# Performance work log

Measured on AMD Instinct MI355X. Metric: run time of the kernel, lower is better.

## Reference

```python
import jax, jax.numpy as jnp
import numpy as np

B, T, U, V = 8, 512, 128, 128  # batch, frames, label len (U+1 pred steps), vocab incl. blank
BLANK = 0


def setup_inputs() -> dict:
    key = jax.random.key(0)
    k1, k2, k3, k4 = jax.random.split(key, 4)
    logits = jax.random.normal(k1, (B, T, U + 1, V), dtype=jnp.float32)
    y = jax.random.randint(k2, (B, U), 1, V).astype(jnp.int32)  # labels, never blank
    logit_lens = jax.random.randint(k3, (B,), T // 2, T + 1).astype(jnp.int32)
    y_lens = jax.random.randint(k4, (B,), U // 2, U + 1).astype(jnp.int32)
    batch_offset = jnp.cumsum(logit_lens * (y_lens + 1)).astype(jnp.int32)
    return {
        "logits": logits,
        "y": y,
        "logit_lens": logit_lens,
        "y_lens": y_lens,
        "batch_offset": batch_offset,
        "max_f_len": T,
    }


def _combine(e1, e2):
    # log-domain affine recurrence x[u] = logaddexp(x[u-1] + c[u], a[u])
    c1, a1 = e1
    c2, a2 = e2
    return (c1 + c2, jnp.logaddexp(a1 + c2, a2))


def rnnt_loss(logits, y, logit_lens, y_lens, blank_idx):
    Bb, Tt, U1, Vv = logits.shape
    Uu = U1 - 1
    lp = jax.nn.log_softmax(logits, axis=-1)            # [B,T,U+1,V]
    blank = lp[..., blank_idx]                          # [B,T,U+1]
    idx = jnp.broadcast_to(y[:, None, :, None], (Bb, Tt, Uu, 1)).astype(jnp.int32)
    emit = jnp.take_along_axis(lp[:, :, :Uu, :], idx, axis=3)[..., 0]  # [B,T,U]

    # alpha[0,u] = sum_{v<u} emit(0,v)
    row0 = jnp.concatenate(
        [jnp.zeros((Bb, 1), lp.dtype), jnp.cumsum(emit[:, 0, :], axis=1)], axis=1
    )  # [B,U+1]
    neg = jnp.full((Bb, 1), -jnp.inf, lp.dtype)

    def step(prev_row, x):
        bl_prev, em_t = x                               # [B,U+1], [B,U]
        a = prev_row + bl_prev                          # come-from-below (blank at t-1)
        c = jnp.concatenate([neg, em_t], axis=1)        # come-from-left (emit at t)
        _, row = jax.lax.associative_scan(_combine, (c, a), axis=1)
        return row, row

    xs = (jnp.swapaxes(blank[:, : Tt - 1, :], 0, 1), jnp.swapaxes(emit[:, 1:, :], 0, 1))
    _, rows = jax.lax.scan(step, row0, xs)              # [T-1,B,U+1]
    alphas = jnp.swapaxes(jnp.concatenate([row0[None], rows], axis=0), 0, 1)  # [B,T,U+1]

    bi = jnp.arange(Bb)
    ti = logit_lens - 1
    ui = y_lens
    ll = alphas[bi, ti, ui] + blank[bi, ti, ui]
    return -ll                                          # per-utterance negative log-lik


def reference(logits, y, logit_lens, y_lens, batch_offset, max_f_len):
    # batch_offset / max_f_len are packing metadata, unused when packed_input=False
    return rnnt_loss(logits, y, logit_lens, y_lens, BLANK).mean()
```

## Files before the change

kernel.cpp:

```cpp
#include <hip/hip_runtime.h>

#define Bb 8
#define Tt 512
#define Uu 128
#define U1 129
#define Vv 128

#define OUT_OFF 0
#define CTROWS 321
#define PCKROW 512
#define PCKBSZ ((size_t)CTROWS * PCKROW)
#define PCK_OFF ((size_t)Bb * Tt * U1 * 2)
#define CTCOL_OFF (PCK_OFF + (size_t)Bb * PCKBSZ)
#define RES_OFF (CTCOL_OFF + (size_t)Bb * CTROWS * 4)

#define K_LN2    0.6931471805599453f
#define K_INVLN2 1.4426950408889634f
#define SENT (-1.0e30f)

__device__ __forceinline__ float fexp2(float x) {
    float r; asm("v_exp_f32 %0, %1" : "=v"(r) : "v"(x)); return r;
}
__device__ __forceinline__ float flog2(float x) {
    float r; asm("v_log_f32 %0, %1" : "=v"(r) : "v"(x)); return r;
}
__device__ __forceinline__ float fmax3(float x, float y, float z) {
    float r; asm("v_max3_f32 %0, %1, %2, %3" : "=v"(r) : "v"(x), "v"(y), "v"(z));
    return r;
}

__global__ __launch_bounds__(256) void lse_kernel(
    const float* __restrict__ logits, const int* __restrict__ y,
    const int* __restrict__ logit_lens, const int* __restrict__ y_lens,
    float* __restrict__ ws)
{
    const int b = blockIdx.y;
    const int t = blockIdx.x;
    if (t >= logit_lens[b]) return;
    const int Ue = y_lens[b];

    float2* outv = (float2*)(ws + OUT_OFF);
    const int wid  = threadIdx.x >> 6;
    const int lane = threadIdx.x & 63;
    const int g    = lane >> 4;
    const int gl   = lane & 15;
    const unsigned rowbase = ((unsigned)b * Tt + t) * U1;
    const int yb = b * Uu;

    for (int u0 = wid * 8; u0 <= Ue; u0 += 32) {
        const int ua = u0 + g;
        const int ub = u0 + 4 + g;
        const int uca = ua > Ue ? Ue : ua;
        const int ucb = ub > Ue ? Ue : ub;
        const float* pa = logits + (size_t)(rowbase + uca) * Vv;
        const float* pb = logits + (size_t)(rowbase + ucb) * Vv;
        float4 a1 = *(const float4*)(pa + gl * 4);
        float4 a2 = *(const float4*)(pa + 64 + gl * 4);
        float4 b1 = *(const float4*)(pb + gl * 4);
        float4 b2 = *(const float4*)(pb + 64 + gl * 4);

        float sa = (fexp2(a1.x * K_INVLN2) + fexp2(a1.y * K_INVLN2))
                 + (fexp2(a1.z * K_INVLN2) + fexp2(a1.w * K_INVLN2))
                 + (fexp2(a2.x * K_INVLN2) + fexp2(a2.y * K_INVLN2))
                 + (fexp2(a2.z * K_INVLN2) + fexp2(a2.w * K_INVLN2));
        float sb = (fexp2(b1.x * K_INVLN2) + fexp2(b1.y * K_INVLN2))
                 + (fexp2(b1.z * K_INVLN2) + fexp2(b1.w * K_INVLN2))
                 + (fexp2(b2.x * K_INVLN2) + fexp2(b2.y * K_INVLN2))
                 + (fexp2(b2.z * K_INVLN2) + fexp2(b2.w * K_INVLN2));
        #pragma unroll
        for (int off = 8; off; off >>= 1) {
            sa += __shfl_xor(sa, off);
            sb += __shfl_xor(sb, off);
        }
        float lseA = flog2(sa);
        float lseB = flog2(sb);

        float emA = SENT, emB = SENT;
        if (uca < Uu) {
            int yv = y[yb + uca];
            int c = yv & 3;
            float4 cv = (yv & 64) ? a2 : a1;
            float cand = (c == 0) ? cv.x : (c == 1) ? cv.y : (c == 2) ? cv.z : cv.w;
            float ev = __shfl(cand, (lane & 48) | ((yv & 63) >> 2));
            emA = ev * K_INVLN2 - lseA;
        }
        if (ucb < Uu) {
            int yv = y[yb + ucb];
            int c = yv & 3;
            float4 cv = (yv & 64) ? b2 : b1;
            float cand = (c == 0) ? cv.x : (c == 1) ? cv.y : (c == 2) ? cv.z : cv.w;
            float ev = __shfl(cand, (lane & 48) | ((yv & 63) >> 2));
            emB = ev * K_INVLN2 - lseB;
        }
        if (gl == 0) {
            if (ua <= Ue) outv[rowbase + ua] = make_float2(a1.x * K_INVLN2 - lseA, emA);
            if (ub <= Ue) outv[rowbase + ub] = make_float2(b1.x * K_INVLN2 - lseB, emB);
        }
    }
}

__device__ __forceinline__ float lae2(float x, float y) {
    float dd = x - y;
    float nad = __builtin_bit_cast(float, __builtin_bit_cast(int, dd) | 0x80000000);
    return fmaxf(x, y) + flog2(1.0f + fexp2(nad));
}
__device__ __forceinline__ float lae3(float x, float y, float z) {
    float m = fmax3(x, y, z);
    return m + flog2(fexp2(x - m) + fexp2(y - m) + fexp2(z - m));
}

__global__ __launch_bounds__(256) void cond_kernel(
    const int* __restrict__ logit_lens, const int* __restrict__ y_lens,
    float* __restrict__ ws)
{
    const int b = blockIdx.x / 320;
    const int m = blockIdx.x - b * 320 + 1;
    if (m > ((logit_lens[b] - 1 + y_lens[b]) >> 1)) return;
    const int r1 = 2 * m - 2, r2 = 2 * m - 1;
    const float2* outv = (const float2*)(ws + OUT_OFF);

    __shared__ float2 D1[U1], D2[U1];
    __shared__ float pckS[PCKROW];
    for (int q = threadIdx.x; q < 2 * U1; q += 256) {
        const int which = q >= U1;
        const int j = q - which * U1;
        const int t = (which ? r2 : r1) - j;
        float2 val = make_float2(SENT, SENT);
        if (t >= 0 && t < Tt) val = outv[((size_t)b * Tt + t) * U1 + j];
        (which ? D2 : D1)[j] = val;
    }
    __syncthreads();

    const int u = threadIdx.x;
    if (u <= 128) {
        float2 d1  = D1[u], d2 = D2[u];
        float2 d1m = (u >= 1) ? D1[u - 1] : make_float2(SENT, SENT);
        float d2my  = (u >= 1) ? D2[u - 1].y : SENT;
        float d1m2y = (u >= 2) ? D1[u - 2].y : SENT;
        float A = d1.x + d2.x;
        float B = lae2(d1m.y + d2.x, d1m.x + d2my);
        float C = d1m2y + d2my;
        if (u < 128) {
            int base = (u >> 1) * 8 + (u & 1);
            pckS[base]     = A;
            pckS[base + 2] = B;
            pckS[base + 4] = C;
            if ((u & 1) == 0) { pckS[base + 6] = 0.0f; pckS[base + 7] = 0.0f; }
        } else {
            ((float4*)(ws + CTCOL_OFF))[(size_t)b * CTROWS + m] = make_float4(A, B, C, 0.0f);
        }
    }
    __syncthreads();

    float* pckG = ws + PCK_OFF + (size_t)b * PCKBSZ + (size_t)m * PCKROW;
    for (int i = threadIdx.x; i < PCKROW; i += 256) pckG[i] = pckS[i];
}

template<int MODE>
__device__ __forceinline__ float rot1(float x, int lane) {
    if constexpr (MODE == 2) {
        float s = __shfl_up(x, 1);
        float w = __shfl(x, 63);
        return (lane == 0) ? w : s;
    } else {
        constexpr int CTRL = (MODE == 0) ? 0x13C : 0x134;
        int i = __builtin_bit_cast(int, x);
        i = __builtin_amdgcn_update_dpp(i, i, CTRL, 0xF, 0xF, true);
        return __builtin_bit_cast(float, i);
    }
}

template<int MODE, bool H128>
__device__ __forceinline__ void dp_body(int b, int lane, int Tb, int Ub,
                                        float* __restrict__ ws)
{
    const float2* outv = (const float2*)(ws + OUT_OFF);
    const float* PCKb = ws + PCK_OFF + (size_t)b * PCKBSZ;
    const float4* COLb = (const float4*)(ws + CTCOL_OFF) + (size_t)b * CTROWS;
    int zv; asm volatile("v_mov_b32 %0, 0" : "=v"(zv));

    float px = (lane == 0) ? 0.0f : SENT;
    float py = SENT, p2 = SENT;
    const int dend = Tb - 1 + Ub;
    const int np   = dend >> 1;
    const int odd  = dend & 1;

    float2 F1 = make_float2(0,0), F2 = make_float2(0,0), G = make_float2(0,0);
    if (odd) {
        const int r = dend - 1;
        int j1 = 2 * lane, j2 = 2 * lane + 1;
        int t1 = r - j1; t1 = t1 > Tt - 1 ? Tt - 1 : t1;
        int t2 = r - j2; t2 = t2 > Tt - 1 ? Tt - 1 : t2;
        F1 = outv[((size_t)b * Tt + t1) * U1 + j1];
        F2 = outv[((size_t)b * Tt + t2) * U1 + j2];
        if constexpr (H128) G = outv[((size_t)b * Tt + (r - 128)) * U1 + 128];
    }
    float pbf = outv[((size_t)b * Tt + (Tb - 1)) * U1 + Ub + zv].x;

    float4 Q0,Q1,Q2,Q3,Q4,Q5,Q6,Q7,Q8,Q9,Q10,Q11,Q12,Q13,Q14,Q15;
    float2 R0,R1,R2,R3,R4,R5,R6,R7,R8,R9,R10,R11,R12,R13,R14,R15;
    float4 O0,O1,O2,O3,O4,O5,O6,O7,O8,O9,O10,O11,O12,O13,O14,O15;

#define LOADC(i, mm) { unsigned o = (unsigned)(mm) * PCKROW + (lane << 3); \
    Q##i = *(const float4*)(PCKb + o); \
    R##i = *(const float2*)(PCKb + o + 4); \
    if constexpr (H128) O##i = COLb[(mm) + zv]; }

#define PIN(i) if constexpr (H128) { \
        asm volatile("" : "+v"(Q##i.x), "+v"(Q##i.y), "+v"(Q##i.z), "+v"(Q##i.w), \
                          "+v"(R##i.x), "+v"(R##i.y), "+v"(O##i.x), "+v"(O##i.y), "+v"(O##i.z)); \
    } else { \
        asm volatile("" : "+v"(Q##i.x), "+v"(Q##i.y), "+v"(Q##i.z), "+v"(Q##i.w), \
                          "+v"(R##i.x), "+v"(R##i.y)); \
    }

#define COMP2(i) { \
    float pm1 = rot1<MODE>(py, lane); \
    float pm0 = rot1<MODE>(px, lane); \
    float nx = lae3(px + Q##i.x, pm1 + Q##i.z, pm0 + R##i.x); \
    float ny = lae3(py + Q##i.y, px + Q##i.w, pm1 + R##i.y); \
    if constexpr (H128) p2 = lae3(p2 + O##i.x, pm1 + O##i.y, pm0 + O##i.z); \
    px = nx; py = ny; }

    LOADC(0,1)   LOADC(1,2)   LOADC(2,3)   LOADC(3,4)
    LOADC(4,5)   LOADC(5,6)   LOADC(6,7)   LOADC(7,8)
    LOADC(8,9)   LOADC(9,10)  LOADC(10,11) LOADC(11,12)
    LOADC(12,13) LOADC(13,14) LOADC(14,15) LOADC(15,16)

    int m = 1;
    for (; m + 15 <= np; m += 16) {
        PIN(0)  COMP2(0)  { int dn = m + 16 > np ? np : m + 16; LOADC(0,  dn) }
        PIN(1)  COMP2(1)  { int dn = m + 17 > np ? np : m + 17; LOADC(1,  dn) }
        PIN(2)  COMP2(2)  { int dn = m + 18 > np ? np : m + 18; LOADC(2,  dn) }
        PIN(3)  COMP2(3)  { int dn = m + 19 > np ? np : m + 19; LOADC(3,  dn) }
        PIN(4)  COMP2(4)  { int dn = m + 20 > np ? np : m + 20; LOADC(4,  dn) }
        PIN(5)  COMP2(5)  { int dn = m + 21 > np ? np : m + 21; LOADC(5,  dn) }
        PIN(6)  COMP2(6)  { int dn = m + 22 > np ? np : m + 22; LOADC(6,  dn) }
        PIN(7)  COMP2(7)  { int dn = m + 23 > np ? np : m + 23; LOADC(7,  dn) }
        PIN(8)  COMP2(8)  { int dn = m + 24 > np ? np : m + 24; LOADC(8,  dn) }
        PIN(9)  COMP2(9)  { int dn = m + 25 > np ? np : m + 25; LOADC(9,  dn) }
        PIN(10) COMP2(10) { int dn = m + 26 > np ? np : m + 26; LOADC(10, dn) }
        PIN(11) COMP2(11) { int dn = m + 27 > np ? np : m + 27; LOADC(11, dn) }
        PIN(12) COMP2(12) { int dn = m + 28 > np ? np : m + 28; LOADC(12, dn) }
        PIN(13) COMP2(13) { int dn = m + 29 > np ? np : m + 29; LOADC(13, dn) }
        PIN(14) COMP2(14) { int dn = m + 30 > np ? np : m + 30; LOADC(14, dn) }
        PIN(15) COMP2(15) { int dn = m + 31 > np ? np : m + 31; LOADC(15, dn) }
    }
#define TAILC(i) if (m <= np) { PIN(i) COMP2(i) m++; }
    TAILC(0)  TAILC(1)  TAILC(2)  TAILC(3)  TAILC(4)
    TAILC(5)  TAILC(6)  TAILC(7)  TAILC(8)  TAILC(9)
    TAILC(10) TAILC(11) TAILC(12) TAILC(13) TAILC(14)

    if (odd) {
        float pm  = rot1<MODE>(py, lane);
        float pmE = rot1<MODE>(F2.y, lane);
        float pmE0 = (lane == 0) ? SENT : pmE;
        float nx = lae2(px + F1.x, pm + pmE0);
        float ny = lae2(py + F2.x, px + F1.y);
        if constexpr (H128) p2 = lae2(p2 + G.x, pm + pmE);
        px = nx; py = ny;
    }

    float a;
    if constexpr (H128) {
        a = __shfl(p2, 0);
    } else {
        float ax = __shfl(px, Ub >> 1);
        float ay = __shfl(py, Ub >> 1);
        a = (Ub & 1) ? ay : ax;
    }
    if (lane == 0) {
        ws[RES_OFF + b] = -(a + pbf) * K_LN2;
    }
#undef LOADC
#undef PIN
#undef COMP2
#undef TAILC
}

__global__ __launch_bounds__(64) void dp_kernel(
    const int* __restrict__ logit_lens, const int* __restrict__ y_lens,
    float* __restrict__ ws)
{
    const int b = blockIdx.x;
    const int lane = threadIdx.x;
    const int Tb = logit_lens[b];
    const int Ub = y_lens[b];
    const bool h = (Ub == 128);
    int li = lane;
    int r0 = __builtin_amdgcn_update_dpp(li, li, 0x13C , 0xF, 0xF, true);
    int r1 = __builtin_amdgcn_update_dpp(li, li, 0x134 , 0xF, 0xF, true);
    int want = (lane + 63) & 63;
    if (__all(r0 == want)) {
        if (h) dp_body<0, true>(b, lane, Tb, Ub, ws);
        else   dp_body<0, false>(b, lane, Tb, Ub, ws);
    } else if (__all(r1 == want)) {
        if (h) dp_body<1, true>(b, lane, Tb, Ub, ws);
        else   dp_body<1, false>(b, lane, Tb, Ub, ws);
    } else {
        if (h) dp_body<2, true>(b, lane, Tb, Ub, ws);
        else   dp_body<2, false>(b, lane, Tb, Ub, ws);
    }
}

__global__ void mean_kernel(const float* __restrict__ res, float* __restrict__ out)
{
    if (threadIdx.x == 0) {
        float s = 0.0f;
        #pragma unroll
        for (int i = 0; i < Bb; ++i) s += res[i];
        out[0] = s * (1.0f / Bb);
    }
}

extern "C" void kernel_launch(void* const* d_in, const int* in_sizes, int n_in,
                              void* d_out, int out_size, void* d_ws, size_t ws_size,
                              hipStream_t stream) {
    const float* logits     = (const float*)d_in[0];
    const int*   y          = (const int*)d_in[1];
    const int*   logit_lens = (const int*)d_in[2];
    const int*   y_lens     = (const int*)d_in[3];
    float* ws  = (float*)d_ws;
    float* out = (float*)d_out;

    dim3 lgrid(Tt, Bb);
    lse_kernel<<<lgrid, 256, 0, stream>>>(logits, y, logit_lens, y_lens, ws);
    cond_kernel<<<Bb * 320, 256, 0, stream>>>(logit_lens, y_lens, ws);
    dp_kernel<<<Bb, 64, 0, stream>>>(logit_lens, y_lens, ws);
    mean_kernel<<<1, 64, 0, stream>>>(ws + RES_OFF, out);
}
```

Before: 69.45 us.

## Compose pairs of diagonal transition matrices to halve serial DP steps

Adds a compose_kernel that multiplies consecutive pairs of banded two-diagonal transition operators in the log-semiring, producing a five-band operator per four anti-diagonals. The serial single-wave DP then advances four diagonals per step using lae5 and two-lane rotations instead of two diagonals with lae3, which shortens the latency-bound sequential chain. In exchange it adds another kernel launch, more workspace traffic and more per-step transcendental work, and the tail handling now covers leftover two-diagonal and odd steps.

```diff
diff --git a/kernel.cpp b/kernel.cpp
--- a/kernel.cpp
+++ b/kernel.cpp
@@ -12,7 +12,12 @@
 #define PCKBSZ ((size_t)CTROWS * PCKROW)
 #define PCK_OFF ((size_t)Bb * Tt * U1 * 2)
 #define CTCOL_OFF (PCK_OFF + (size_t)Bb * PCKBSZ)
-#define RES_OFF (CTCOL_OFF + (size_t)Bb * CTROWS * 4)
+#define WROWF 768
+#define WROWS 160
+#define WBSZ ((size_t)WROWS * WROWF)
+#define W_OFF (CTCOL_OFF + (size_t)Bb * CTROWS * 4)
+#define WCOL_OFF (W_OFF + (size_t)Bb * WBSZ)
+#define RES_OFF (WCOL_OFF + (size_t)Bb * WROWS * 8)
 
 #define K_LN2    0.6931471805599453f
 #define K_INVLN2 1.4426950408889634f
@@ -107,6 +112,12 @@
 __device__ __forceinline__ float lae3(float x, float y, float z) {
     float m = fmax3(x, y, z);
     return m + flog2(fexp2(x - m) + fexp2(y - m) + fexp2(z - m));
+}
+__device__ __forceinline__ float lae5(float a, float b, float c, float d, float e) {
+    float m = fmax3(a, b, c);
+    m = fmax3(m, d, e);
+    return m + flog2(fexp2(a - m) + fexp2(b - m) + fexp2(c - m)
+                   + fexp2(d - m) + fexp2(e - m));
 }
 
 __global__ __launch_bounds__(256) void cond_kernel(
@@ -156,6 +167,70 @@
     for (int i = threadIdx.x; i < PCKROW; i += 256) pckG[i] = pckS[i];
 }
 
+__global__ __launch_bounds__(256) void compose_kernel(
+    const int* __restrict__ logit_lens, const int* __restrict__ y_lens,
+    float* __restrict__ ws)
+{
+    const int b = blockIdx.x / 159;
+    const int q = blockIdx.x - b * 159 + 1;
+    const int dend = logit_lens[b] - 1 + y_lens[b];
+    if (4 * q > dend) return;
+    const int m1 = 2 * q - 1, m2 = 2 * q;
+    const float* PCKb = ws + PCK_OFF + (size_t)b * PCKBSZ;
+    const float4* COLb = (const float4*)(ws + CTCOL_OFF) + (size_t)b * CTROWS;
+
+    __shared__ float a1s[131], b1s[131], c1s[131];
+    __shared__ float wrk[WROWF];
+    const int u = threadIdx.x;
+    if (u < 2) { a1s[u] = SENT; b1s[u] = SENT; c1s[u] = SENT; }
+    if (u < 128) {
+        const float* p = PCKb + (size_t)m1 * PCKROW + (u >> 1) * 8;
+        int par = u & 1;
+        a1s[u + 2] = p[par]; b1s[u + 2] = p[2 + par]; c1s[u + 2] = p[4 + par];
+    } else if (u == 128) {
+        float4 cc = COLb[m1];
+        a1s[130] = cc.x; b1s[130] = cc.y; c1s[130] = cc.z;
+    }
+    __syncthreads();
+
+    if (u <= 128) {
+        float A2, B2, C2;
+        if (u < 128) {
+            const float* p = PCKb + (size_t)m2 * PCKROW + (u >> 1) * 8;
+            int par = u & 1;
+            A2 = p[par]; B2 = p[2 + par]; C2 = p[4 + par];
+        } else {
+            float4 cc = COLb[m2];
+            A2 = cc.x; B2 = cc.y; C2 = cc.z;
+        }
+        float A1 = a1s[u + 2], A1m = a1s[u + 1], A1m2 = a1s[u];
+        float B1 = b1s[u + 2], B1m = b1s[u + 1], B1m2 = b1s[u];
+        float C1 = c1s[u + 2], C1m = c1s[u + 1], C1m2 = c1s[u];
+        float W0 = A2 + A1;
+        float W1 = lae2(A2 + B1, B2 + A1m);
+        float W2 = lae3(A2 + C1, B2 + B1m, C2 + A1m2);
+        float W3 = lae2(B2 + C1m, C2 + B1m2);
+        float W4 = C2 + C1m2;
+        if (u < 128) {
+            int base = (u >> 1) * 12 + (u & 1);
+            wrk[base]     = W0;
+            wrk[base + 2] = W1;
+            wrk[base + 4] = W2;
+            wrk[base + 6] = W3;
+            wrk[base + 8] = W4;
+            if ((u & 1) == 0) { wrk[base + 10] = 0.0f; wrk[base + 11] = 0.0f; }
+        } else {
+            float* wc = ws + WCOL_OFF + ((size_t)b * WROWS + q) * 8;
+            wc[0] = W0; wc[1] = W1; wc[2] = W2; wc[3] = W3; wc[4] = W4;
+            wc[5] = 0.0f; wc[6] = 0.0f; wc[7] = 0.0f;
+        }
+    }
+    __syncthreads();
+
+    float* wg = ws + W_OFF + (size_t)b * WBSZ + (size_t)q * WROWF;
+    for (int i = threadIdx.x; i < WROWF; i += 256) wg[i] = wrk[i];
+}
+
 template<int MODE>
 __device__ __forceinline__ float rot1(float x, int lane) {
     if constexpr (MODE == 2) {
@@ -177,16 +252,24 @@
     const float2* outv = (const float2*)(ws + OUT_OFF);
     const float* PCKb = ws + PCK_OFF + (size_t)b * PCKBSZ;
     const float4* COLb = (const float4*)(ws + CTCOL_OFF) + (size_t)b * CTROWS;
+    const float* WTb = ws + W_OFF + (size_t)b * WBSZ;
+    const float* WCb = ws + WCOL_OFF + (size_t)b * WROWS * 8;
     int zv; asm volatile("v_mov_b32 %0, 0" : "=v"(zv));
 
     float px = (lane == 0) ? 0.0f : SENT;
     float py = SENT, p2 = SENT;
     const int dend = Tb - 1 + Ub;
-    const int np   = dend >> 1;
-    const int odd  = dend & 1;
+    const int nq   = dend >> 2;
+    const int rem  = dend & 3;
+
+    const int mpair = 2 * nq + 1;
+    float4 Qp = *(const float4*)(PCKb + (size_t)mpair * PCKROW + (lane << 3));
+    float2 Rp = *(const float2*)(PCKb + (size_t)mpair * PCKROW + (lane << 3) + 4);
+    float4 Op = make_float4(SENT, SENT, SENT, 0.0f);
+    if constexpr (H128) Op = COLb[mpair + zv];
 
     float2 F1 = make_float2(0,0), F2 = make_float2(0,0), G = make_float2(0,0);
-    if (odd) {
+    if (rem & 1) {
         const int r = dend - 1;
         int j1 = 2 * lane, j2 = 2 * lane + 1;
         int t1 = r - j1; t1 = t1 > Tt - 1 ? Tt - 1 : t1;
@@ -197,61 +280,69 @@
     }
     float pbf = outv[((size_t)b * Tt + (Tb - 1)) * U1 + Ub + zv].x;
 
-    float4 Q0,Q1,Q2,Q3,Q4,Q5,Q6,Q7,Q8,Q9,Q10,Q11,Q12,Q13,Q14,Q15;
-    float2 R0,R1,R2,R3,R4,R5,R6,R7,R8,R9,R10,R11,R12,R13,R14,R15;
-    float4 O0,O1,O2,O3,O4,O5,O6,O7,O8,O9,O10,O11,O12,O13,O14,O15;
-
-#define LOADC(i, mm) { unsigned o = (unsigned)(mm) * PCKROW + (lane << 3); \
-    Q##i = *(const float4*)(PCKb + o); \
-    R##i = *(const float2*)(PCKb + o + 4); \
-    if constexpr (H128) O##i = COLb[(mm) + zv]; }
+    float4 A0,A1,A2,A3,A4,A5,A6,A7;
+    float4 B0,B1,B2,B3,B4,B5,B6,B7;
+    float2 C0,C1,C2,C3,C4,C5,C6,C7;
+    float4 Oa0,Oa1,Oa2,Oa3,Oa4,Oa5,Oa6,Oa7;
+    float2 Oc0,Oc1,Oc2,Oc3,Oc4,Oc5,Oc6,Oc7;
+
+#define LOADW(i, qq) { unsigned o = (unsigned)(qq) * WROWF + lane * 12; \
+    A##i = *(const float4*)(WTb + o); \
+    B##i = *(const float4*)(WTb + o + 4); \
+    C##i = *(const float2*)(WTb + o + 8); \
+    if constexpr (H128) { \
+        Oa##i = *(const float4*)(WCb + (qq) * 8 + zv); \
+        Oc##i = *(const float2*)(WCb + (qq) * 8 + 4 + zv); } }
 
 #define PIN(i) if constexpr (H128) { \
-        asm volatile("" : "+v"(Q##i.x), "+v"(Q##i.y), "+v"(Q##i.z), "+v"(Q##i.w), \
-                          "+v"(R##i.x), "+v"(R##i.y), "+v"(O##i.x), "+v"(O##i.y), "+v"(O##i.z)); \
+        asm volatile("" : "+v"(A##i.x), "+v"(A##i.y), "+v"(A##i.z), "+v"(A##i.w), \
+                          "+v"(B##i.x), "+v"(B##i.y), "+v"(B##i.z), "+v"(B##i.w), \
+                          "+v"(C##i.x), "+v"(C##i.y), \
+                          "+v"(Oa##i.x), "+v"(Oa##i.y), "+v"(Oa##i.z), "+v"(Oa##i.w), \
+                          "+v"(Oc##i.x)); \
     } else { \
-        asm volatile("" : "+v"(Q##i.x), "+v"(Q##i.y), "+v"(Q##i.z), "+v"(Q##i.w), \
-                          "+v"(R##i.x), "+v"(R##i.y)); \
-    }
-
-#define COMP2(i) { \
-    float pm1 = rot1<MODE>(py, lane); \
-    float pm0 = rot1<MODE>(px, lane); \
-    float nx = lae3(px + Q##i.x, pm1 + Q##i.z, pm0 + R##i.x); \
-    float ny = lae3(py + Q##i.y, px + Q##i.w, pm1 + R##i.y); \
-    if constexpr (H128) p2 = lae3(p2 + O##i.x, pm1 + O##i.y, pm0 + O##i.z); \
+        asm volatile("" : "+v"(A##i.x), "+v"(A##i.y), "+v"(A##i.z), "+v"(A##i.w), \
+                          "+v"(B##i.x), "+v"(B##i.y), "+v"(B##i.z), "+v"(B##i.w), \
+                          "+v"(C##i.x), "+v"(C##i.y)); \
+    }
+
+#define COMP4(i) { \
+    float p1y = rot1<MODE>(py, lane); \
+    float p1x = rot1<MODE>(px, lane); \
+    float p2y = rot1<MODE>(p1y, lane); \
+    float p2x = rot1<MODE>(p1x, lane); \
+    float nx = lae5(px + A##i.x, p1y + A##i.z, p1x + B##i.x, p2y + B##i.z, p2x + C##i.x); \
+    float ny = lae5(py + A##i.y, px + A##i.w, p1y + B##i.y, p1x + B##i.w, p2y + C##i.y); \
+    if constexpr (H128) p2 = lae5(p2 + Oa##i.x, p1y + Oa##i.y, p1x + Oa##i.z, \
+                                  p2y + Oa##i.w, p2x + Oc##i.x); \
     px = nx; py = ny; }
 
-    LOADC(0,1)   LOADC(1,2)   LOADC(2,3)   LOADC(3,4)
-    LOADC(4,5)   LOADC(5,6)   LOADC(6,7)   LOADC(7,8)
-    LOADC(8,9)   LOADC(9,10)  LOADC(10,11) LOADC(11,12)
-    LOADC(12,13) LOADC(13,14) LOADC(14,15) LOADC(15,16)
-
-    int m = 1;
-    for (; m + 15 <= np; m += 16) {
-        PIN(0)  COMP2(0)  { int dn = m + 16 > np ? np : m + 16; LOADC(0,  dn) }
-        PIN(1)  COMP2(1)  { int dn = m + 17 > np ? np : m + 17; LOADC(1,  dn) }
-        PIN(2)  COMP2(2)  { int dn = m + 18 > np ? np : m + 18; LOADC(2,  dn) }
-        PIN(3)  COMP2(3)  { int dn = m + 19 > np ? np : m + 19; LOADC(3,  dn) }
-        PIN(4)  COMP2(4)  { int dn = m + 20 > np ? np : m + 20; LOADC(4,  dn) }
-        PIN(5)  COMP2(5)  { int dn = m + 21 > np ? np : m + 21; LOADC(5,  dn) }
-        PIN(6)  COMP2(6)  { int dn = m + 22 > np ? np : m + 22; LOADC(6,  dn) }
-        PIN(7)  COMP2(7)  { int dn = m + 23 > np ? np : m + 23; LOADC(7,  dn) }
-        PIN(8)  COMP2(8)  { int dn = m + 24 > np ? np : m + 24; LOADC(8,  dn) }
-        PIN(9)  COMP2(9)  { int dn = m + 25 > np ? np : m + 25; LOADC(9,  dn) }
-        PIN(10) COMP2(10) { int dn = m + 26 > np ? np : m + 26; LOADC(10, dn) }
-        PIN(11) COMP2(11) { int dn = m + 27 > np ? np : m + 27; LOADC(11, dn) }
-        PIN(12) COMP2(12) { int dn = m + 28 > np ? np : m + 28; LOADC(12, dn) }
-        PIN(13) COMP2(13) { int dn = m + 29 > np ? np : m + 29; LOADC(13, dn) }
-        PIN(14) COMP2(14) { int dn = m + 30 > np ? np : m + 30; LOADC(14, dn) }
-        PIN(15) COMP2(15) { int dn = m + 31 > np ? np : m + 31; LOADC(15, dn) }
-    }
-#define TAILC(i) if (m <= np) { PIN(i) COMP2(i) m++; }
-    TAILC(0)  TAILC(1)  TAILC(2)  TAILC(3)  TAILC(4)
-    TAILC(5)  TAILC(6)  TAILC(7)  TAILC(8)  TAILC(9)
-    TAILC(10) TAILC(11) TAILC(12) TAILC(13) TAILC(14)
-
-    if (odd) {
+    LOADW(0,1) LOADW(1,2) LOADW(2,3) LOADW(3,4)
+    LOADW(4,5) LOADW(5,6) LOADW(6,7) LOADW(7,8)
+
+    int q = 1;
+    for (; q + 7 <= nq; q += 8) {
+        PIN(0) COMP4(0) { int dn = q + 8  > nq ? nq : q + 8;  LOADW(0, dn) }
+        PIN(1) COMP4(1) { int dn = q + 9  > nq ? nq : q + 9;  LOADW(1, dn) }
+        PIN(2) COMP4(2) { int dn = q + 10 > nq ? nq : q + 10; LOADW(2, dn) }
+        PIN(3) COMP4(3) { int dn = q + 11 > nq ? nq : q + 11; LOADW(3, dn) }
+        PIN(4) COMP4(4) { int dn = q + 12 > nq ? nq : q + 12; LOADW(4, dn) }
+        PIN(5) COMP4(5) { int dn = q + 13 > nq ? nq : q + 13; LOADW(5, dn) }
+        PIN(6) COMP4(6) { int dn = q + 14 > nq ? nq : q + 14; LOADW(6, dn) }
+        PIN(7) COMP4(7) { int dn = q + 15 > nq ? nq : q + 15; LOADW(7, dn) }
+    }
+#define TAILW(i) if (q <= nq) { PIN(i) COMP4(i) q++; }
+    TAILW(0) TAILW(1) TAILW(2) TAILW(3) TAILW(4) TAILW(5) TAILW(6)
+
+    if (rem >= 2) {
+        float pm1 = rot1<MODE>(py, lane);
+        float pm0 = rot1<MODE>(px, lane);
+        float nx = lae3(px + Qp.x, pm1 + Qp.z, pm0 + Rp.x);
+        float ny = lae3(py + Qp.y, px + Qp.w, pm1 + Rp.y);
+        if constexpr (H128) p2 = lae3(p2 + Op.x, pm1 + Op.y, pm0 + Op.z);
+        px = nx; py = ny;
+    }
+    if (rem & 1) {
         float pm  = rot1<MODE>(py, lane);
         float pmE = rot1<MODE>(F2.y, lane);
         float pmE0 = (lane == 0) ? SENT : pmE;
@@ -272,10 +363,10 @@
     if (lane == 0) {
         ws[RES_OFF + b] = -(a + pbf) * K_LN2;
     }
-#undef LOADC
+#undef LOADW
 #undef PIN
-#undef COMP2
-#undef TAILC
+#undef COMP4
+#undef TAILW
 }
 
 __global__ __launch_bounds__(64) void dp_kernel(
@@ -326,6 +417,7 @@
     dim3 lgrid(Tt, Bb);
     lse_kernel<<<lgrid, 256, 0, stream>>>(logits, y, logit_lens, y_lens, ws);
     cond_kernel<<<Bb * 320, 256, 0, stream>>>(logit_lens, y_lens, ws);
+    compose_kernel<<<Bb * 159, 256, 0, stream>>>(logit_lens, y_lens, ws);
     dp_kernel<<<Bb, 64, 0, stream>>>(logit_lens, y_lens, ws);
     mean_kernel<<<1, 64, 0, stream>>>(ws + RES_OFF, out);
 }
```

Result: no change. 68.73 us (median of 2 runs) (-1.0%).

## Process four diagonal pairs per lane exchange in RNNT alpha DP

Applied to the files above, without the earlier changes.

Reworks the serial DP so each lane keeps a 10-wide window of alpha values and advances four anti-diagonal pairs (eight diagonals) between cross-lane exchanges. Previously every pair step needed DPP rotations. The precompute kernel now emits per-group packed coefficient records laid out for coalesced float4 loads, and the DPP-mode dispatch is dropped in favour of plain shuffles. The aim is to cut cross-lane communication latency on the serial critical path. The cost is redundant overlapping work per lane, more registers, and a more complex precompute.

```diff
diff --git a/kernel.cpp b/kernel.cpp
--- a/kernel.cpp
+++ b/kernel.cpp
@@ -7,12 +7,13 @@
 #define Vv 128
 
 #define OUT_OFF 0
-#define CTROWS 321
-#define PCKROW 512
-#define PCKBSZ ((size_t)CTROWS * PCKROW)
-#define PCK_OFF ((size_t)Bb * Tt * U1 * 2)
-#define CTCOL_OFF (PCK_OFF + (size_t)Bb * PCKBSZ)
-#define RES_OFF (CTCOL_OFF + (size_t)Bb * CTROWS * 4)
+#define NGRP 80
+#define GRECROWF 4096
+#define GRECBSZ ((size_t)NGRP * GRECROWF)
+#define GREC_OFF ((size_t)Bb * Tt * U1 * 2)
+#define GCOLSTR 1284
+#define GCOL_OFF (GREC_OFF + (size_t)Bb * GRECBSZ)
+#define RES_OFF (GCOL_OFF + (size_t)Bb * GCOLSTR)
 
 #define K_LN2    0.6931471805599453f
 #define K_INVLN2 1.4426950408889634f
@@ -27,6 +28,15 @@
 __device__ __forceinline__ float fmax3(float x, float y, float z) {
     float r; asm("v_max3_f32 %0, %1, %2, %3" : "=v"(r) : "v"(x), "v"(y), "v"(z));
     return r;
+}
+__device__ __forceinline__ float lae2(float x, float y) {
+    float dd = x - y;
+    float nad = __builtin_bit_cast(float, __builtin_bit_cast(int, dd) | 0x80000000);
+    return fmaxf(x, y) + flog2(1.0f + fexp2(nad));
+}
+__device__ __forceinline__ float lae3(float x, float y, float z) {
+    float m = fmax3(x, y, z);
+    return m + flog2(fexp2(x - m) + fexp2(y - m) + fexp2(z - m));
 }
 
 __global__ __launch_bounds__(256) void lse_kernel(
@@ -99,94 +109,121 @@
     }
 }
 
-__device__ __forceinline__ float lae2(float x, float y) {
-    float dd = x - y;
-    float nad = __builtin_bit_cast(float, __builtin_bit_cast(int, dd) | 0x80000000);
-    return fmaxf(x, y) + flog2(1.0f + fexp2(nad));
-}
-__device__ __forceinline__ float lae3(float x, float y, float z) {
-    float m = fmax3(x, y, z);
-    return m + flog2(fexp2(x - m) + fexp2(y - m) + fexp2(z - m));
-}
-
-__global__ __launch_bounds__(256) void cond_kernel(
+__global__ __launch_bounds__(256) void gcond_kernel(
     const int* __restrict__ logit_lens, const int* __restrict__ y_lens,
     float* __restrict__ ws)
 {
-    const int b = blockIdx.x / 320;
-    const int m = blockIdx.x - b * 320 + 1;
-    if (m > ((logit_lens[b] - 1 + y_lens[b]) >> 1)) return;
-    const int r1 = 2 * m - 2, r2 = 2 * m - 1;
+    const int b = blockIdx.x / NGRP;
+    const int g = blockIdx.x - b * NGRP + 1;
+    const int np = (logit_lens[b] - 1 + y_lens[b]) >> 1;
+    if (4 * (g - 1) >= np) return;
     const float2* outv = (const float2*)(ws + OUT_OFF);
 
-    __shared__ float2 D1[U1], D2[U1];
-    __shared__ float pckS[PCKROW];
-    for (int q = threadIdx.x; q < 2 * U1; q += 256) {
-        const int which = q >= U1;
-        const int j = q - which * U1;
-        const int t = (which ? r2 : r1) - j;
-        float2 val = make_float2(SENT, SENT);
-        if (t >= 0 && t < Tt) val = outv[((size_t)b * Tt + t) * U1 + j];
-        (which ? D2 : D1)[j] = val;
+    __shared__ float2 Dr[8][U1];
+    __shared__ float ABC[3 * 4 * 136];
+    __shared__ float recS[GRECROWF / NGRP * NGRP / 64];
+    __shared__ float rec[4096];
+
+    const int tid = threadIdx.x;
+    for (int i = tid; i < 8 * U1; i += 256) {
+        int row = i / U1, j = i - row * U1;
+        int r = 8 * (g - 1) + row;
+        int t = r - j;
+        Dr[row][j] = (t >= 0 && t < Tt) ? outv[((size_t)b * Tt + t) * U1 + j]
+                                        : make_float2(SENT, SENT);
     }
     __syncthreads();
 
-    const int u = threadIdx.x;
-    if (u <= 128) {
-        float2 d1  = D1[u], d2 = D2[u];
-        float2 d1m = (u >= 1) ? D1[u - 1] : make_float2(SENT, SENT);
-        float d2my  = (u >= 1) ? D2[u - 1].y : SENT;
-        float d1m2y = (u >= 2) ? D1[u - 2].y : SENT;
+    if (tid < 136) {
+        const int s = tid - 8;
+        #pragma unroll
+        for (int k = 0; k < 4; ++k) {
+            float A = SENT, B = SENT, C = SENT;
+            if (s >= 0) {
+                float2 d1 = Dr[2 * k][s], d2 = Dr[2 * k + 1][s];
+                float2 d1m = (s >= 1) ? Dr[2 * k][s - 1] : make_float2(SENT, SENT);
+                float d2my  = (s >= 1) ? Dr[2 * k + 1][s - 1].y : SENT;
+                float d1m2y = (s >= 2) ? Dr[2 * k][s - 2].y : SENT;
+                A = d1.x + d2.x;
+                B = lae2(d1m.y + d2.x, d1m.x + d2my);
+                C = d1m2y + d2my;
+            }
+            ABC[k * 136 + tid]        = A;
+            ABC[544 + k * 136 + tid]  = B;
+            ABC[1088 + k * 136 + tid] = C;
+        }
+    } else if (tid >= 160 && tid < 164) {
+        const int k = tid - 160;
+        float2 d1 = Dr[2 * k][128], d2 = Dr[2 * k + 1][128];
+        float2 d1m = Dr[2 * k][127];
+        float d2my  = Dr[2 * k + 1][127].y;
+        float d1m2y = Dr[2 * k][126].y;
         float A = d1.x + d2.x;
         float B = lae2(d1m.y + d2.x, d1m.x + d2my);
         float C = d1m2y + d2my;
-        if (u < 128) {
-            int base = (u >> 1) * 8 + (u & 1);
-            pckS[base]     = A;
-            pckS[base + 2] = B;
-            pckS[base + 4] = C;
-            if ((u & 1) == 0) { pckS[base + 6] = 0.0f; pckS[base + 7] = 0.0f; }
-        } else {
-            ((float4*)(ws + CTCOL_OFF))[(size_t)b * CTROWS + m] = make_float4(A, B, C, 0.0f);
-        }
+        ((float4*)(ws + GCOL_OFF))[(size_t)b * (GCOLSTR / 4) + 4 * (g - 1) + k + 1]
+            = make_float4(A, B, C, 0.0f);
     }
     __syncthreads();
 
-    float* pckG = ws + PCK_OFF + (size_t)b * PCKBSZ + (size_t)m * PCKROW;
-    for (int i = threadIdx.x; i < PCKROW; i += 256) pckG[i] = pckS[i];
-}
-
-template<int MODE>
-__device__ __forceinline__ float rot1(float x, int lane) {
-    if constexpr (MODE == 2) {
-        float s = __shfl_up(x, 1);
-        float w = __shfl(x, 63);
-        return (lane == 0) ? w : s;
-    } else {
-        constexpr int CTRL = (MODE == 0) ? 0x13C : 0x134;
-        int i = __builtin_bit_cast(int, x);
-        i = __builtin_amdgcn_update_dpp(i, i, CTRL, 0xF, 0xF, true);
-        return __builtin_bit_cast(float, i);
-    }
-}
-
-template<int MODE, bool H128>
+    if (tid < 64) {
+        const int l = tid, i2 = 2 * l, base = l * 64;
+        const int offA[4] = {0, 24, 42, 54}, offB[4] = {8, 30, 46, 56},
+                  offC[4] = {16, 36, 50, 58}, jlo[4] = {2, 4, 6, 8};
+        #pragma unroll
+        for (int k = 0; k < 4; ++k) {
+            const float* As = ABC + k * 136;
+            const float* Bs = ABC + 544 + k * 136;
+            const float* Cs = ABC + 1088 + k * 136;
+            for (int j = jlo[k]; j <= 9; ++j) {
+                rec[base + offA[k] + j - jlo[k]] = As[i2 + j];
+                rec[base + offB[k] + j - jlo[k]] = Bs[i2 + j];
+                rec[base + offC[k] + j - jlo[k]] = Cs[i2 + j];
+            }
+        }
+        rec[base + 60] = 0.0f; rec[base + 61] = 0.0f;
+        rec[base + 62] = 0.0f; rec[base + 63] = 0.0f;
+    }
+    __syncthreads();
+
+    float4* out4 = (float4*)(ws + GREC_OFF) + (size_t)b * (GRECBSZ / 4)
+                 + (size_t)(g - 1) * 1024;
+    const float4* rec4 = (const float4*)rec;
+    for (int i = tid; i < 1024; i += 256) {
+        int q = i >> 6, l = i & 63;
+        out4[i] = rec4[l * 16 + q];
+    }
+}
+
+template<bool H128>
 __device__ __forceinline__ void dp_body(int b, int lane, int Tb, int Ub,
                                         float* __restrict__ ws)
 {
     const float2* outv = (const float2*)(ws + OUT_OFF);
-    const float* PCKb = ws + PCK_OFF + (size_t)b * PCKBSZ;
-    const float4* COLb = (const float4*)(ws + CTCOL_OFF) + (size_t)b * CTROWS;
+    const float4* GREC4 = (const float4*)(ws + GREC_OFF) + (size_t)b * (GRECBSZ / 4);
+    const float4* GCOL4 = (const float4*)(ws + GCOL_OFF) + (size_t)b * (GCOLSTR / 4);
     int zv; asm volatile("v_mov_b32 %0, 0" : "=v"(zv));
 
-    float px = (lane == 0) ? 0.0f : SENT;
-    float py = SENT, p2 = SENT;
     const int dend = Tb - 1 + Ub;
     const int np   = dend >> 1;
-    const int odd  = dend & 1;
+    const int ng   = np >> 2;
+    const int lv   = np & 3;
+    const int rem  = dend & 1;
+    const int gmax = (np + 3) >> 2;
+
+    float w0,w1,w2,w3,w4,w5,w6,w7,w8,w9;
+    {
+        int s0 = 2 * lane - 8;
+        w0=(s0==0)?0.0f:SENT;   w1=(s0+1==0)?0.0f:SENT;
+        w2=(s0+2==0)?0.0f:SENT; w3=(s0+3==0)?0.0f:SENT;
+        w4=(s0+4==0)?0.0f:SENT; w5=(s0+5==0)?0.0f:SENT;
+        w6=(s0+6==0)?0.0f:SENT; w7=(s0+7==0)?0.0f:SENT;
+        w8=(s0+8==0)?0.0f:SENT; w9=(s0+9==0)?0.0f:SENT;
+    }
+    float w128 = SENT;
 
     float2 F1 = make_float2(0,0), F2 = make_float2(0,0), G = make_float2(0,0);
-    if (odd) {
+    if (rem) {
         const int r = dend - 1;
         int j1 = 2 * lane, j2 = 2 * lane + 1;
         int t1 = r - j1; t1 = t1 > Tt - 1 ? Tt - 1 : t1;
@@ -197,85 +234,125 @@
     }
     float pbf = outv[((size_t)b * Tt + (Tb - 1)) * U1 + Ub + zv].x;
 
-    float4 Q0,Q1,Q2,Q3,Q4,Q5,Q6,Q7,Q8,Q9,Q10,Q11,Q12,Q13,Q14,Q15;
-    float2 R0,R1,R2,R3,R4,R5,R6,R7,R8,R9,R10,R11,R12,R13,R14,R15;
-    float4 O0,O1,O2,O3,O4,O5,O6,O7,O8,O9,O10,O11,O12,O13,O14,O15;
-
-#define LOADC(i, mm) { unsigned o = (unsigned)(mm) * PCKROW + (lane << 3); \
-    Q##i = *(const float4*)(PCKb + o); \
-    R##i = *(const float2*)(PCKb + o + 4); \
-    if constexpr (H128) O##i = COLb[(mm) + zv]; }
-
-#define PIN(i) if constexpr (H128) { \
-        asm volatile("" : "+v"(Q##i.x), "+v"(Q##i.y), "+v"(Q##i.z), "+v"(Q##i.w), \
-                          "+v"(R##i.x), "+v"(R##i.y), "+v"(O##i.x), "+v"(O##i.y), "+v"(O##i.z)); \
-    } else { \
-        asm volatile("" : "+v"(Q##i.x), "+v"(Q##i.y), "+v"(Q##i.z), "+v"(Q##i.w), \
-                          "+v"(R##i.x), "+v"(R##i.y)); \
-    }
-
-#define COMP2(i) { \
-    float pm1 = rot1<MODE>(py, lane); \
-    float pm0 = rot1<MODE>(px, lane); \
-    float nx = lae3(px + Q##i.x, pm1 + Q##i.z, pm0 + R##i.x); \
-    float ny = lae3(py + Q##i.y, px + Q##i.w, pm1 + R##i.y); \
-    if constexpr (H128) p2 = lae3(p2 + O##i.x, pm1 + O##i.y, pm0 + O##i.z); \
-    px = nx; py = ny; }
-
-    LOADC(0,1)   LOADC(1,2)   LOADC(2,3)   LOADC(3,4)
-    LOADC(4,5)   LOADC(5,6)   LOADC(6,7)   LOADC(7,8)
-    LOADC(8,9)   LOADC(9,10)  LOADC(10,11) LOADC(11,12)
-    LOADC(12,13) LOADC(13,14) LOADC(14,15) LOADC(15,16)
-
-    int m = 1;
-    for (; m + 15 <= np; m += 16) {
-        PIN(0)  COMP2(0)  { int dn = m + 16 > np ? np : m + 16; LOADC(0,  dn) }
-        PIN(1)  COMP2(1)  { int dn = m + 17 > np ? np : m + 17; LOADC(1,  dn) }
-        PIN(2)  COMP2(2)  { int dn = m + 18 > np ? np : m + 18; LOADC(2,  dn) }
-        PIN(3)  COMP2(3)  { int dn = m + 19 > np ? np : m + 19; LOADC(3,  dn) }
-        PIN(4)  COMP2(4)  { int dn = m + 20 > np ? np : m + 20; LOADC(4,  dn) }
-        PIN(5)  COMP2(5)  { int dn = m + 21 > np ? np : m + 21; LOADC(5,  dn) }
-        PIN(6)  COMP2(6)  { int dn = m + 22 > np ? np : m + 22; LOADC(6,  dn) }
-        PIN(7)  COMP2(7)  { int dn = m + 23 > np ? np : m + 23; LOADC(7,  dn) }
-        PIN(8)  COMP2(8)  { int dn = m + 24 > np ? np : m + 24; LOADC(8,  dn) }
-        PIN(9)  COMP2(9)  { int dn = m + 25 > np ? np : m + 25; LOADC(9,  dn) }
-        PIN(10) COMP2(10) { int dn = m + 26 > np ? np : m + 26; LOADC(10, dn) }
-        PIN(11) COMP2(11) { int dn = m + 27 > np ? np : m + 27; LOADC(11, dn) }
-        PIN(12) COMP2(12) { int dn = m + 28 > np ? np : m + 28; LOADC(12, dn) }
-        PIN(13) COMP2(13) { int dn = m + 29 > np ? np : m + 29; LOADC(13, dn) }
-        PIN(14) COMP2(14) { int dn = m + 30 > np ? np : m + 30; LOADC(14, dn) }
-        PIN(15) COMP2(15) { int dn = m + 31 > np ? np : m + 31; LOADC(15, dn) }
-    }
-#define TAILC(i) if (m <= np) { PIN(i) COMP2(i) m++; }
-    TAILC(0)  TAILC(1)  TAILC(2)  TAILC(3)  TAILC(4)
-    TAILC(5)  TAILC(6)  TAILC(7)  TAILC(8)  TAILC(9)
-    TAILC(10) TAILC(11) TAILC(12) TAILC(13) TAILC(14)
-
-    if (odd) {
-        float pm  = rot1<MODE>(py, lane);
-        float pmE = rot1<MODE>(F2.y, lane);
-        float pmE0 = (lane == 0) ? SENT : pmE;
-        float nx = lae2(px + F1.x, pm + pmE0);
-        float ny = lae2(py + F2.x, px + F1.y);
-        if constexpr (H128) p2 = lae2(p2 + G.x, pm + pmE);
-        px = nx; py = ny;
+    float4 QA[16], QB[16], CLA[4], CLB[4];
+
+#define LOADG(Q, CL, gg) { \
+    const float4* P = GREC4 + (size_t)((gg) - 1) * 1024 + lane; \
+    _Pragma("unroll") \
+    for (int q = 0; q < 16; ++q) Q[q] = P[q * 64]; \
+    if constexpr (H128) { \
+        int m0 = 4 * ((gg) - 1) + 1 + zv; \
+        CL[0] = GCOL4[m0]; CL[1] = GCOL4[m0 + 1]; \
+        CL[2] = GCOL4[m0 + 2]; CL[3] = GCOL4[m0 + 3]; } }
+
+#define PINQ(Q, CL) { \
+    asm volatile("" : "+v"(Q[0].x),  "+v"(Q[1].x),  "+v"(Q[2].x),  "+v"(Q[3].x), \
+                      "+v"(Q[4].x),  "+v"(Q[5].x),  "+v"(Q[6].x),  "+v"(Q[7].x)); \
+    asm volatile("" : "+v"(Q[8].x),  "+v"(Q[9].x),  "+v"(Q[10].x), "+v"(Q[11].x), \
+                      "+v"(Q[12].x), "+v"(Q[13].x), "+v"(Q[14].x), "+v"(Q[15].x)); \
+    if constexpr (H128) \
+        asm volatile("" : "+v"(CL[0].x), "+v"(CL[1].x), "+v"(CL[2].x), "+v"(CL[3].x)); }
+
+#define STEP1(Q, CL) { float nw = SENT; \
+    if constexpr (H128) nw = lae3(w128 + CL[0].x, w9 + CL[0].y, w8 + CL[0].z); \
+    w9 = lae3(w9 + Q[1].w, w8 + Q[3].w, w7 + Q[5].w); \
+    w8 = lae3(w8 + Q[1].z, w7 + Q[3].z, w6 + Q[5].z); \
+    w7 = lae3(w7 + Q[1].y, w6 + Q[3].y, w5 + Q[5].y); \
+    w6 = lae3(w6 + Q[1].x, w5 + Q[3].x, w4 + Q[5].x); \
+    w5 = lae3(w5 + Q[0].w, w4 + Q[2].w, w3 + Q[4].w); \
+    w4 = lae3(w4 + Q[0].z, w3 + Q[2].z, w2 + Q[4].z); \
+    w3 = lae3(w3 + Q[0].y, w2 + Q[2].y, w1 + Q[4].y); \
+    w2 = lae3(w2 + Q[0].x, w1 + Q[2].x, w0 + Q[4].x); \
+    if constexpr (H128) w128 = nw; }
+
+#define STEP2(Q, CL) { float nw = SENT; \
+    if constexpr (H128) nw = lae3(w128 + CL[1].x, w9 + CL[1].y, w8 + CL[1].z); \
+    w9 = lae3(w9 + Q[7].y, w8 + Q[8].w, w7 + Q[10].y); \
+    w8 = lae3(w8 + Q[7].x, w7 + Q[8].z, w6 + Q[10].x); \
+    w7 = lae3(w7 + Q[6].w, w6 + Q[8].y, w5 + Q[9].w); \
+    w6 = lae3(w6 + Q[6].z, w5 + Q[8].x, w4 + Q[9].z); \
+    w5 = lae3(w5 + Q[6].y, w4 + Q[7].w, w3 + Q[9].y); \
+    w4 = lae3(w4 + Q[6].x, w3 + Q[7].z, w2 + Q[9].x); \
+    if constexpr (H128) w128 = nw; }
+
+#define STEP3(Q, CL) { float nw = SENT; \
+    if constexpr (H128) nw = lae3(w128 + CL[2].x, w9 + CL[2].y, w8 + CL[2].z); \
+    w9 = lae3(w9 + Q[11].y, w8 + Q[12].y, w7 + Q[13].y); \
+    w8 = lae3(w8 + Q[11].x, w7 + Q[12].x, w6 + Q[13].x); \
+    w7 = lae3(w7 + Q[10].w, w6 + Q[11].w, w5 + Q[12].w); \
+    w6 = lae3(w6 + Q[10].z, w5 + Q[11].z, w4 + Q[12].z); \
+    if constexpr (H128) w128 = nw; }
+
+#define STEP4(Q, CL) { float nw = SENT; \
+    if constexpr (H128) nw = lae3(w128 + CL[3].x, w9 + CL[3].y, w8 + CL[3].z); \
+    w9 = lae3(w9 + Q[13].w, w8 + Q[14].y, w7 + Q[14].w); \
+    w8 = lae3(w8 + Q[13].z, w7 + Q[14].x, w6 + Q[14].z); \
+    if constexpr (H128) w128 = nw; }
+
+#define EXCHG() { \
+    float n0 = __shfl(w8, lane - 4), n1 = __shfl(w9, lane - 4); \
+    float n2 = __shfl(w8, lane - 3), n3 = __shfl(w9, lane - 3); \
+    float n4 = __shfl(w8, lane - 2), n5 = __shfl(w9, lane - 2); \
+    float n6 = __shfl(w8, lane - 1), n7 = __shfl(w9, lane - 1); \
+    int l2 = 2 * lane; \
+    w0 = (l2 < 8) ? SENT : n0;     w1 = (l2 + 1 < 8) ? SENT : n1; \
+    w2 = (l2 + 2 < 8) ? SENT : n2; w3 = (l2 + 3 < 8) ? SENT : n3; \
+    w4 = (l2 + 4 < 8) ? SENT : n4; w5 = (l2 + 5 < 8) ? SENT : n5; \
+    w6 = (l2 + 6 < 8) ? SENT : n6; w7 = (l2 + 7 < 8) ? SENT : n7; }
+
+#define GROUPX(Q, CL) { STEP1(Q, CL) STEP2(Q, CL) STEP3(Q, CL) STEP4(Q, CL) EXCHG() }
+
+    LOADG(QA, CLA, 1)
+    LOADG(QB, CLB, (2 > gmax ? gmax : 2))
+
+    int g = 1;
+    for (; g + 1 <= ng; g += 2) {
+        PINQ(QA, CLA) GROUPX(QA, CLA)
+        { int dn = g + 2 > gmax ? gmax : g + 2; LOADG(QA, CLA, dn) }
+        PINQ(QB, CLB) GROUPX(QB, CLB)
+        { int dn = g + 3 > gmax ? gmax : g + 3; LOADG(QB, CLB, dn) }
+    }
+    if (g <= ng) { PINQ(QA, CLA) GROUPX(QA, CLA) }
+
+    if (lv) {
+        LOADG(QA, CLA, gmax)
+        PINQ(QA, CLA)
+        STEP1(QA, CLA)
+        if (lv >= 2) STEP2(QA, CLA)
+        if (lv >= 3) STEP3(QA, CLA)
+    }
+
+    if (rem) {
+        float aL  = __shfl(w9, lane - 1);
+        float emL = __shfl(F2.y, lane - 1);
+        float nw = SENT;
+        if constexpr (H128)
+            nw = lae2(w128 + G.x, w9 + F2.y);
+        float nx = lae2(w8 + F1.x, (lane == 0) ? SENT : aL + emL);
+        float ny = lae2(w9 + F2.x, w8 + F1.y);
+        w8 = nx; w9 = ny;
+        if constexpr (H128) w128 = nw;
     }
 
     float a;
     if constexpr (H128) {
-        a = __shfl(p2, 0);
+        a = __shfl(w128, 63);
     } else {
-        float ax = __shfl(px, Ub >> 1);
-        float ay = __shfl(py, Ub >> 1);
+        float ax = __shfl(w8, Ub >> 1);
+        float ay = __shfl(w9, Ub >> 1);
         a = (Ub & 1) ? ay : ax;
     }
     if (lane == 0) {
         ws[RES_OFF + b] = -(a + pbf) * K_LN2;
     }
-#undef LOADC
-#undef PIN
-#undef COMP2
-#undef TAILC
+#undef LOADG
+#undef PINQ
+#undef STEP1
+#undef STEP2
+#undef STEP3
+#undef STEP4
+#undef EXCHG
+#undef GROUPX
 }
 
 __global__ __launch_bounds__(64) void dp_kernel(
@@ -286,21 +363,8 @@
     const int lane = threadIdx.x;
     const int Tb = logit_lens[b];
     const int Ub = y_lens[b];
-    const bool h = (Ub == 128);
-    int li = lane;
-    int r0 = __builtin_amdgcn_update_dpp(li, li, 0x13C , 0xF, 0xF, true);
-    int r1 = __builtin_amdgcn_update_dpp(li, li, 0x134 , 0xF, 0xF, true);
-    int want = (lane + 63) & 63;
-    if (__all(r0 == want)) {
-        if (h) dp_body<0, true>(b, lane, Tb, Ub, ws);
-        else   dp_body<0, false>(b, lane, Tb, Ub, ws);
-    } else if (__all(r1 == want)) {
-        if (h) dp_body<1, true>(b, lane, Tb, Ub, ws);
-        else   dp_body<1, false>(b, lane, Tb, Ub, ws);
-    } else {
-        if (h) dp_body<2, true>(b, lane, Tb, Ub, ws);
-        else   dp_body<2, false>(b, lane, Tb, Ub, ws);
-    }
+    if (Ub == 128) dp_body<true>(b, lane, Tb, Ub, ws);
+    else           dp_body<false>(b, lane, Tb, Ub, ws);
 }
 
 __global__ void mean_kernel(const float* __restrict__ res, float* __restrict__ out)
@@ -325,7 +389,7 @@
 
     dim3 lgrid(Tt, Bb);
     lse_kernel<<<lgrid, 256, 0, stream>>>(logits, y, logit_lens, y_lens, ws);
-    cond_kernel<<<Bb * 320, 256, 0, stream>>>(logit_lens, y_lens, ws);
+    gcond_kernel<<<Bb * NGRP, 256, 0, stream>>>(logit_lens, y_lens, ws);
     dp_kernel<<<Bb, 64, 0, stream>>>(logit_lens, y_lens, ws);
     mean_kernel<<<1, 64, 0, stream>>>(ws + RES_OFF, out);
 }
```

Result: slower. 102.8 us (+48.0%).
